# Kernel tuning notes

Measured on AMD Instinct MI355X. Metric: run time of the kernel, lower is better.

Reference implementation:

```python
import jax, jax.numpy as jnp
import numpy as np

B, P, ENC = 64, 196, 512
E, H, A, V, L = 1024, 1024, 512, 20000, 25


def setup_inputs() -> dict:
    key = jax.random.key(0)
    ks = jax.random.split(key, 20)
    s = 0.02
    return {
        "encoder_out": jax.random.normal(ks[0], (B, P, ENC), jnp.float32),
        "captions": jax.random.randint(ks[1], (B, L), 0, V),
        "lengths": L,
        # attention MLP
        "W_enc_att": jax.random.normal(ks[2], (ENC, A), jnp.float32) * s,
        "b_enc_att": jnp.zeros((A,), jnp.float32),
        "W_dec_att": jax.random.normal(ks[3], (H, A), jnp.float32) * s,
        "b_dec_att": jnp.zeros((A,), jnp.float32),
        "W_full_att": jax.random.normal(ks[4], (A, 1), jnp.float32) * s,
        "b_full_att": jnp.zeros((1,), jnp.float32),
        # embedding
        "emb_table": jax.random.normal(ks[5], (V, E), jnp.float32) * s,
        # LSTMCell: input = embedding + context -> (E+ENC, 4H)
        "W_ih": jax.random.normal(ks[6], (E + ENC, 4 * H), jnp.float32) * s,
        "b_ih": jnp.zeros((4 * H,), jnp.float32),
        "W_hh": jax.random.normal(ks[7], (H, 4 * H), jnp.float32) * s,
        "b_hh": jnp.zeros((4 * H,), jnp.float32),
        # init states
        "W_init_h": jax.random.normal(ks[8], (ENC, H), jnp.float32) * s,
        "b_init_h": jnp.zeros((H,), jnp.float32),
        "W_init_c": jax.random.normal(ks[9], (ENC, H), jnp.float32) * s,
        "b_init_c": jnp.zeros((H,), jnp.float32),
        # gate + output proj
        "W_fbeta": jax.random.normal(ks[10], (H, ENC), jnp.float32) * s,
        "b_fbeta": jnp.zeros((ENC,), jnp.float32),
        "W_fc": jax.random.normal(ks[11], (H, V), jnp.float32) * s,
        "b_fc": jnp.zeros((V,), jnp.float32),
    }


def _decode(encoder_out, W_enc_att, b_enc_att, W_dec_att, b_dec_att,
            W_full_att, b_full_att, emb_table, W_ih, b_ih, W_hh, b_hh,
            W_init_h, b_init_h, W_init_c, b_init_c, W_fbeta, b_fbeta,
            W_fc, b_fc, captions, T):
    # precompute encoder-side attention projection (constant across timesteps)
    att_enc = encoder_out @ W_enc_att + b_enc_att          # (B, P, A)
    mean_feat = encoder_out.mean(axis=1)                   # (B, ENC)
    h0 = mean_feat @ W_init_h + b_init_h
    c0 = mean_feat @ W_init_c + b_init_c
    embeddings = emb_table[captions[:, :T]]                # (B, T, E)
    xs = jnp.swapaxes(embeddings, 0, 1)                    # (T, B, E)

    def step(carry, emb_t):
        h, c = carry
        att_dec = h @ W_dec_att + b_dec_att                # (B, A)
        energy = (jax.nn.relu(att_enc + att_dec[:, None, :]) @ W_full_att
                  + b_full_att)[..., 0]                    # (B, P)
        alpha = jax.nn.softmax(energy, axis=1)
        context = jnp.einsum('bp,bpe->be', alpha, encoder_out)
        gate = jax.nn.sigmoid(h @ W_fbeta + b_fbeta)       # (B, ENC)
        x = jnp.concatenate([emb_t, gate * context], axis=1)
        gates = x @ W_ih + b_ih + h @ W_hh + b_hh          # (B, 4H)
        i, f, g, o = jnp.split(gates, 4, axis=1)           # torch order i,f,g,o
        c = jax.nn.sigmoid(f) * c + jax.nn.sigmoid(i) * jnp.tanh(g)
        h = jax.nn.sigmoid(o) * jnp.tanh(c)
        preds = h @ W_fc + b_fc                            # dropout = identity (eval)
        return (h, c), (preds, alpha)

    _, (preds, alphas) = jax.lax.scan(step, (h0, c0), xs)
    predictions = jnp.swapaxes(preds, 0, 1)                # (B, T, V)
    alphas = jnp.swapaxes(alphas, 0, 1)                    # (B, T, P)
    return predictions, alphas


def reference(encoder_out, captions, lengths, W_enc_att, b_enc_att, W_dec_att,
              b_dec_att, W_full_att, b_full_att, emb_table, W_ih, b_ih, W_hh,
              b_hh, W_init_h, b_init_h, W_init_c, b_init_c, W_fbeta, b_fbeta,
              W_fc, b_fc):
    T = int(lengths) - 1
    return _decode(encoder_out, W_enc_att, b_enc_att, W_dec_att, b_dec_att,
                   W_full_att, b_full_att, emb_table, W_ih, b_ih, W_hh, b_hh,
                   W_init_h, b_init_h, W_init_c, b_init_c, W_fbeta, b_fbeta,
                   W_fc, b_fc, captions, T)
```

## Files before the change

kernel.cpp:

```cpp
#include <hip/hip_runtime.h>
#include <hip/hip_bf16.h>

#define BB 64
#define PP 196
#define ENCD 512
#define ED 1024
#define HD 1024
#define AD 512
#define VD 20000
#define TT 24
#define VPAD 20096
#define NS 8

typedef __attribute__((ext_vector_type(8))) short short8;
typedef __attribute__((ext_vector_type(4))) short short4v;
typedef __attribute__((ext_vector_type(4))) float f32x4;

__device__ __forceinline__ unsigned short f2bf(float f) {
    unsigned u = __builtin_bit_cast(unsigned, f);
    u = (u + 0x7FFFu + ((u >> 16) & 1u)) >> 16;
    return (unsigned short)u;
}
__device__ __forceinline__ void split2(float v, unsigned short& h, unsigned short& l) {
    h = f2bf(v);
    float hf = __builtin_bit_cast(float, ((unsigned)h) << 16);
    l = f2bf(v - hf);
}

__global__ __launch_bounds__(256) void split_w_kernel(
    const float* __restrict__ W, unsigned short* __restrict__ oh,
    unsigned short* __restrict__ ol, int N, int Npad, int coff, int Nlaunch) {
    int n = blockIdx.x * 256 + threadIdx.x;
    if (n >= Nlaunch) return;
    int kc = blockIdx.y;
    short8 vh, vl;
    #pragma unroll
    for (int j = 0; j < 8; ++j) {
        float v = (n < N) ? W[(size_t)(kc * 8 + j) * N + n] : 0.f;
        unsigned short h, l; split2(v, h, l);
        vh[j] = (short)h; vl[j] = (short)l;
    }
    size_t o = ((size_t)kc * Npad + coff + n) * 8;
    *(short8*)(oh + o) = vh; *(short8*)(ol + o) = vl;
}

__global__ __launch_bounds__(128) void embed_split_kernel(
    const int* __restrict__ captions, const float* __restrict__ table,
    unsigned short* __restrict__ eh, unsigned short* __restrict__ el) {
    int t = blockIdx.x, b = blockIdx.y;
    int kc = threadIdx.x;
    int tok = captions[b * 25 + t];
    const float* row = table + (size_t)tok * ED;
    short8 vh, vl;
    #pragma unroll
    for (int j = 0; j < 8; ++j) {
        unsigned short h, l; split2(row[kc * 8 + j], h, l);
        vh[j] = (short)h; vl[j] = (short)l;
    }
    size_t o = ((size_t)t * 128 * 64 + (size_t)kc * 64 + b) * 8;
    *(short8*)(eh + o) = vh; *(short8*)(el + o) = vl;
}

__global__ __launch_bounds__(512) void mean_kernel(const float* __restrict__ enc,
                                                   float* __restrict__ mf) {
    int b = blockIdx.x; int e = threadIdx.x;
    const float* base = enc + (size_t)b * PP * ENCD + e;
    float s = 0.f;
    #pragma unroll 4
    for (int p = 0; p < PP; ++p) s += base[(size_t)p * ENCD];
    mf[b * ENCD + e] = s * (1.f / PP);
}

__global__ __launch_bounds__(256) void init_hc_kernel(
    const float* __restrict__ mf,
    const float* __restrict__ Wh, const float* __restrict__ bh,
    const float* __restrict__ Wc, const float* __restrict__ bc,
    unsigned short* __restrict__ hc_h, unsigned short* __restrict__ hc_l,
    float* __restrict__ c0) {
    int b = blockIdx.x;
    int isC = blockIdx.y;
    const float* W    = isC ? Wc : Wh;
    const float* bias = isC ? bc : bh;
    __shared__ float smf[ENCD];
    for (int i = threadIdx.x; i < ENCD; i += 256) smf[i] = mf[b * ENCD + i];
    __syncthreads();
    #pragma unroll
    for (int jj = 0; jj < 4; ++jj) {
        int j = threadIdx.x + jj * 256;
        float acc = bias[j];
        for (int k = 0; k < ENCD; ++k) acc += smf[k] * W[(size_t)k * HD + j];
        if (isC) c0[b * HD + j] = acc;
        else {
            unsigned short h, l; split2(acc, h, l);
            size_t o = ((size_t)(j >> 3) * 64 + b) * 8 + (j & 7);
            hc_h[o] = h; hc_l[o] = l;
        }
    }
}

__global__ __launch_bounds__(256) void mfma_gemm_bigf(
    const float* __restrict__ Ap,
    const unsigned short* __restrict__ Bh, const unsigned short* __restrict__ Bl,
    const float* __restrict__ bias, float* __restrict__ C,
    int N, int Npad, int K, int Mtiles, int Ntiles, int inner_m) {
    __shared__ __align__(16) short lds[32768];
    short* Ahs = lds;
    short* Als = lds + 8192;
    short* Bhs = lds + 16384;
    short* Bls = lds + 24576;
    int tid = threadIdx.x, lane = tid & 63, w = tid >> 6;
    int nwg = Mtiles * Ntiles;
    int orig = blockIdx.x;
    int q = nwg >> 3, r = nwg & 7;
    int xcd = orig & 7;
    int basew = (xcd < r) ? xcd * (q + 1) : r * (q + 1) + (xcd - r) * q;
    int wg = basew + (orig >> 3);
    int mt, nt;
    if (inner_m) { mt = wg % Mtiles; nt = wg / Mtiles; }
    else         { nt = wg % Ntiles; mt = wg / Ntiles; }
    int m0 = mt * 128, n0 = nt * 128;
    int wr = w >> 1, wc = w & 1;
    f32x4 acc[4][4];
    #pragma unroll
    for (int i = 0; i < 4; ++i)
        #pragma unroll
        for (int j = 0; j < 4; ++j) acc[i][j] = (f32x4){0.f, 0.f, 0.f, 0.f};
    int nsteps = K >> 6;
    for (int s = 0; s < nsteps; ++s) {
        int k0 = s * 64, kc0 = s * 8;
        float4 va[8];
        #pragma unroll
        for (int it = 0; it < 8; ++it) {
            int idx = it * 256 + tid; int m = idx >> 4, k4 = idx & 15;
            va[it] = *(const float4*)(Ap + (size_t)(m0 + m) * K + k0 + k4 * 4);
        }
        short8 rb[2][4];
        #pragma unroll
        for (int it = 0; it < 4; ++it) {
            int g = w * 4 + it; int kcl = g >> 1; int rb0 = (g & 1) * 64;
            size_t gb = ((size_t)(kc0 + kcl) * Npad + n0 + rb0 + lane) * 8;
            rb[0][it] = *(const short8*)(Bh + gb);
            rb[1][it] = *(const short8*)(Bl + gb);
        }
        __syncthreads();
        #pragma unroll
        for (int it = 0; it < 8; ++it) {
            int idx = it * 256 + tid; int m = idx >> 4, k4 = idx & 15;
            int kc = k4 >> 1, jh = (k4 & 1) * 4;
            float vv[4] = {va[it].x, va[it].y, va[it].z, va[it].w};
            short4v hv, lv;
            #pragma unroll
            for (int qq = 0; qq < 4; ++qq) {
                unsigned short h, l; split2(vv[qq], h, l);
                hv[qq] = (short)h; lv[qq] = (short)l;
            }
            int o = kc * 1024 + ((m ^ kc) << 3) + jh;
            *(short4v*)(Ahs + o) = hv;
            *(short4v*)(Als + o) = lv;
        }
        #pragma unroll
        for (int it = 0; it < 4; ++it) {
            int g = w * 4 + it; int kcl = g >> 1; int rb0 = (g & 1) * 64;
            int o = (kcl * 128 + rb0 + lane) * 8;
            *(short8*)(Bhs + o) = rb[0][it];
            *(short8*)(Bls + o) = rb[1][it];
        }
        __syncthreads();
        #pragma unroll
        for (int ks = 0; ks < 2; ++ks) {
            int kq = ks * 4 + (lane >> 4);
            short8 afh[4], afl[4], bfh[4], bfl[4];
            #pragma unroll
            for (int mi = 0; mi < 4; ++mi) {
                int row = wr * 64 + mi * 16 + (lane & 15);
                int o = kq * 1024 + ((row ^ kq) << 3);
                afh[mi] = *(const short8*)(Ahs + o);
                afl[mi] = *(const short8*)(Als + o);
            }
            #pragma unroll
            for (int ni = 0; ni < 4; ++ni) {
                int o = (kq * 128 + wc * 64 + ni * 16 + (lane & 15)) * 8;
                bfh[ni] = *(const short8*)(Bhs + o);
                bfl[ni] = *(const short8*)(Bls + o);
            }
            #pragma unroll
            for (int mi = 0; mi < 4; ++mi)
                #pragma unroll
                for (int ni = 0; ni < 4; ++ni) {
                    acc[mi][ni] = __builtin_amdgcn_mfma_f32_16x16x32_bf16(afh[mi], bfh[ni], acc[mi][ni], 0, 0, 0);
                    acc[mi][ni] = __builtin_amdgcn_mfma_f32_16x16x32_bf16(afh[mi], bfl[ni], acc[mi][ni], 0, 0, 0);
                    acc[mi][ni] = __builtin_amdgcn_mfma_f32_16x16x32_bf16(afl[mi], bfh[ni], acc[mi][ni], 0, 0, 0);
                }
        }
    }
    #pragma unroll
    for (int mi = 0; mi < 4; ++mi) {
        int rrow = m0 + wr * 64 + mi * 16 + ((lane >> 4) << 2);
        #pragma unroll
        for (int ni = 0; ni < 4; ++ni) {
            int c = n0 + wc * 64 + ni * 16 + (lane & 15);
            if (c < N) {
                float bv = bias ? bias[c] : 0.f;
                #pragma unroll
                for (int qq = 0; qq < 4; ++qq)
                    C[(size_t)(rrow + qq) * N + c] = acc[mi][ni][qq] + bv;
            }
        }
    }
}

__global__ __launch_bounds__(256) void mfma_gemm_small(
    const unsigned short* __restrict__ A0h, const unsigned short* __restrict__ A0l,
    const unsigned short* __restrict__ A1h, const unsigned short* __restrict__ A1l,
    const unsigned short* __restrict__ A2h, const unsigned short* __restrict__ A2l,
    int c0, int c1,
    const unsigned short* __restrict__ B0h, const unsigned short* __restrict__ B0l,
    const unsigned short* __restrict__ B1h, const unsigned short* __restrict__ B1l,
    int bc0, float* __restrict__ out, int Npad, int steps) {
    __shared__ __align__(16) short lds[24576];
    short* Ahs = lds;
    short* Als = lds + 4096;
    short* Bhs = lds + 8192;
    short* Bls = lds + 16384;
    int tid = threadIdx.x, lane = tid & 63, w = tid >> 6;
    int n0 = blockIdx.x * 128;
    int kc_base = blockIdx.y * steps * 8;
    out += (size_t)blockIdx.y * 64 * Npad;
    f32x4 acc[4][2];
    #pragma unroll
    for (int i = 0; i < 4; ++i)
        #pragma unroll
        for (int j = 0; j < 2; ++j) acc[i][j] = (f32x4){0.f, 0.f, 0.f, 0.f};
    for (int s = 0; s < steps; ++s) {
        int kc0 = kc_base + s * 8;
        short8 raa[2][2], rbb[2][4];
        #pragma unroll
        for (int it = 0; it < 2; ++it) {
            int kcl = w * 2 + it; int kcg = kc0 + kcl;
            const unsigned short *ph, *pl; size_t off;
            if (kcg < c0)       { ph = A0h; pl = A0l; off = ((size_t)kcg * 64 + lane) * 8; }
            else if (kcg < c1)  { ph = A1h; pl = A1l; off = ((size_t)(kcg - c0) * 64 + lane) * 8; }
            else                { ph = A2h; pl = A2l; off = ((size_t)(kcg - c1) * 64 + lane) * 8; }
            raa[0][it] = *(const short8*)(ph + off);
            raa[1][it] = *(const short8*)(pl + off);
        }
        #pragma unroll
        for (int it = 0; it < 4; ++it) {
            int g = w * 4 + it; int kcl = g >> 1; int cb = (g & 1) * 64; int kcg = kc0 + kcl;
            const unsigned short *ph, *pl; size_t off;
            if (kcg < bc0) { ph = B0h; pl = B0l; off = ((size_t)kcg * Npad + n0 + cb + lane) * 8; }
            else           { ph = B1h; pl = B1l; off = ((size_t)(kcg - bc0) * Npad + n0 + cb + lane) * 8; }
            rbb[0][it] = *(const short8*)(ph + off);
            rbb[1][it] = *(const short8*)(pl + off);
        }
        __syncthreads();
        #pragma unroll
        for (int it = 0; it < 2; ++it) {
            int kcl = w * 2 + it; int o = (kcl * 64 + lane) * 8;
            *(short8*)(Ahs + o) = raa[0][it];
            *(short8*)(Als + o) = raa[1][it];
        }
        #pragma unroll
        for (int it = 0; it < 4; ++it) {
            int g = w * 4 + it; int kcl = g >> 1; int cb = (g & 1) * 64;
            int o = (kcl * 128 + cb + lane) * 8;
            *(short8*)(Bhs + o) = rbb[0][it];
            *(short8*)(Bls + o) = rbb[1][it];
        }
        __syncthreads();
        #pragma unroll
        for (int ks = 0; ks < 2; ++ks) {
            int kq = ks * 4 + (lane >> 4);
            short8 afh[4], afl[4], bfh[2], bfl[2];
            #pragma unroll
            for (int mi = 0; mi < 4; ++mi) {
                int o = (kq * 64 + mi * 16 + (lane & 15)) * 8;
                afh[mi] = *(const short8*)(Ahs + o);
                afl[mi] = *(const short8*)(Als + o);
            }
            #pragma unroll
            for (int ni = 0; ni < 2; ++ni) {
                int o = (kq * 128 + w * 32 + ni * 16 + (lane & 15)) * 8;
                bfh[ni] = *(const short8*)(Bhs + o);
                bfl[ni] = *(const short8*)(Bls + o);
            }
            #pragma unroll
            for (int mi = 0; mi < 4; ++mi)
                #pragma unroll
                for (int ni = 0; ni < 2; ++ni) {
                    acc[mi][ni] = __builtin_amdgcn_mfma_f32_16x16x32_bf16(afh[mi], bfh[ni], acc[mi][ni], 0, 0, 0);
                    acc[mi][ni] = __builtin_amdgcn_mfma_f32_16x16x32_bf16(afh[mi], bfl[ni], acc[mi][ni], 0, 0, 0);
                    acc[mi][ni] = __builtin_amdgcn_mfma_f32_16x16x32_bf16(afl[mi], bfh[ni], acc[mi][ni], 0, 0, 0);
                }
        }
        __syncthreads();
    }
    #pragma unroll
    for (int mi = 0; mi < 4; ++mi) {
        int rrow = mi * 16 + ((lane >> 4) << 2);
        #pragma unroll
        for (int ni = 0; ni < 2; ++ni) {
            int c = n0 + w * 32 + ni * 16 + (lane & 15);
            #pragma unroll
            for (int qq = 0; qq < 4; ++qq)
                out[(size_t)(rrow + qq) * Npad + c] = acc[mi][ni][qq];
        }
    }
}

__global__ __launch_bounds__(512) void attn_fused_kernel(
    const float* __restrict__ att_enc, const float* __restrict__ adg,
    const float* __restrict__ b_dec, const float* __restrict__ Wfull,
    const float* __restrict__ enc, const float* __restrict__ b_fbeta,
    float* __restrict__ alpha_out, unsigned short* __restrict__ x2h,
    unsigned short* __restrict__ x2l, int t) {
    int b = blockIdx.x; int tid = threadIdx.x;
    __shared__ float sdec[AD], sw[AD], red[512], sal[PP];
    if (tid < AD) {
        float s = b_dec[tid];
        #pragma unroll
        for (int ks = 0; ks < NS; ++ks) s += adg[((size_t)ks * BB + b) * 1024 + tid];
        sdec[tid] = s;
        sw[tid] = Wfull[tid];
    }
    __syncthreads();
    int p = tid & 255, half = tid >> 8;
    float part = 0.f;
    if (p < PP) {
        const float* row = att_enc + ((size_t)b * PP + p) * AD + half * 256;
        const float* sd = sdec + half * 256;
        const float* swp = sw + half * 256;
        #pragma unroll 4
        for (int a0 = 0; a0 < 256; a0 += 4) {
            float4 v = *(const float4*)(row + a0);
            part += fmaxf(v.x + sd[a0 + 0], 0.f) * swp[a0 + 0];
            part += fmaxf(v.y + sd[a0 + 1], 0.f) * swp[a0 + 1];
            part += fmaxf(v.z + sd[a0 + 2], 0.f) * swp[a0 + 2];
            part += fmaxf(v.w + sd[a0 + 3], 0.f) * swp[a0 + 3];
        }
    }
    red[tid] = part;
    __syncthreads();
    float myE = (tid < PP) ? red[tid] + red[tid + 256] : -1e30f;
    __syncthreads();
    red[tid] = myE;
    __syncthreads();
    for (int s = 256; s > 0; s >>= 1) {
        if (tid < s) red[tid] = fmaxf(red[tid], red[tid + s]);
        __syncthreads();
    }
    float mx = red[0];
    __syncthreads();
    float ex = (tid < PP) ? __expf(myE - mx) : 0.f;
    red[tid] = ex;
    __syncthreads();
    for (int s = 256; s > 0; s >>= 1) {
        if (tid < s) red[tid] += red[tid + s];
        __syncthreads();
    }
    float al = ex * (1.f / red[0]);
    if (tid < PP) {
        sal[tid] = al;
        alpha_out[((size_t)b * TT + t) * PP + tid] = al;
    }
    __syncthreads();
    int e = tid;
    const float* basep = enc + (size_t)b * PP * ENCD + e;
    float s = 0.f;
    #pragma unroll 4
    for (int pp = 0; pp < PP; ++pp) s += sal[pp] * basep[(size_t)pp * ENCD];
    float gpre = b_fbeta[e];
    #pragma unroll
    for (int ks = 0; ks < NS; ++ks) gpre += adg[((size_t)ks * BB + b) * 1024 + AD + e];
    float gate = 1.f / (1.f + __expf(-gpre));
    unsigned short h, l; split2(gate * s, h, l);
    size_t o = ((size_t)(e >> 3) * 64 + b) * 8 + (e & 7);
    x2h[o] = h; x2l[o] = l;
}

__global__ __launch_bounds__(256) void lstm_kernel(
    const float* __restrict__ gp, const float* __restrict__ b_ih,
    const float* __restrict__ b_hh, float* __restrict__ c,
    unsigned short* __restrict__ hc_h, unsigned short* __restrict__ hc_l,
    float* __restrict__ h_all, int t) {
    int b = blockIdx.x; int tid = threadIdx.x;
    #pragma unroll
    for (int jj = 0; jj < 4; ++jj) {
        int j = tid + jj * 256;
        float gi = b_ih[j] + b_hh[j];
        float gf = b_ih[1024 + j] + b_hh[1024 + j];
        float gg = b_ih[2048 + j] + b_hh[2048 + j];
        float go = b_ih[3072 + j] + b_hh[3072 + j];
        #pragma unroll
        for (int ks = 0; ks < NS; ++ks) {
            const float* g = gp + ((size_t)ks * BB + b) * 4096;
            gi += g[j]; gf += g[1024 + j]; gg += g[2048 + j]; go += g[3072 + j];
        }
        float si = 1.f / (1.f + __expf(-gi));
        float sf = 1.f / (1.f + __expf(-gf));
        float so = 1.f / (1.f + __expf(-go));
        float cn = sf * c[b * HD + j] + si * tanhf(gg);
        c[b * HD + j] = cn;
        float hn = so * tanhf(cn);
        unsigned short h, l; split2(hn, h, l);
        size_t o1 = ((size_t)(j >> 3) * 64 + b) * 8 + (j & 7);
        hc_h[o1] = h; hc_l[o1] = l;
        h_all[((size_t)b * TT + t) * HD + j] = hn;
    }
}

extern "C" void kernel_launch(void* const* d_in, const int* in_sizes, int n_in,
                              void* d_out, int out_size, void* d_ws, size_t ws_size,
                              hipStream_t stream) {
    const float* enc      = (const float*)d_in[0];
    const int*   captions = (const int*)d_in[1];
    const float* W_enc    = (const float*)d_in[3];
    const float* b_enc    = (const float*)d_in[4];
    const float* W_dec    = (const float*)d_in[5];
    const float* b_dec    = (const float*)d_in[6];
    const float* W_full   = (const float*)d_in[7];
    const float* table    = (const float*)d_in[9];
    const float* W_ih     = (const float*)d_in[10];
    const float* b_ih     = (const float*)d_in[11];
    const float* W_hh     = (const float*)d_in[12];
    const float* b_hh     = (const float*)d_in[13];
    const float* W_init_h = (const float*)d_in[14];
    const float* b_init_h = (const float*)d_in[15];
    const float* W_init_c = (const float*)d_in[16];
    const float* b_init_c = (const float*)d_in[17];
    const float* W_fbeta  = (const float*)d_in[18];
    const float* b_fbeta  = (const float*)d_in[19];
    const float* W_fc     = (const float*)d_in[20];
    const float* b_fc     = (const float*)d_in[21];

    float* preds  = (float*)d_out;
    float* alphas = (float*)d_out + (size_t)BB * TT * VD;

    char* base = (char*)d_ws;
    size_t off = 0;
    auto take = [&](size_t b) { void* r = (void*)(base + off); off += (b + 255) & ~(size_t)255; return r; };
    float* att_enc = (float*)take((size_t)12544 * 512 * 4);
    unsigned short* wih_h  = (unsigned short*)take((size_t)192 * 4096 * 8 * 2);
    unsigned short* wih_l  = (unsigned short*)take((size_t)192 * 4096 * 8 * 2);
    unsigned short* whh_h  = (unsigned short*)take((size_t)128 * 4096 * 8 * 2);
    unsigned short* whh_l  = (unsigned short*)take((size_t)128 * 4096 * 8 * 2);
    unsigned short* watt_h = (unsigned short*)take((size_t)128 * 1024 * 8 * 2);
    unsigned short* watt_l = (unsigned short*)take((size_t)128 * 1024 * 8 * 2);
    unsigned short* wenc_h = (unsigned short*)take((size_t)64 * 512 * 8 * 2);
    unsigned short* wenc_l = (unsigned short*)take((size_t)64 * 512 * 8 * 2);
    unsigned short* emb_h  = (unsigned short*)take((size_t)TT * 128 * 64 * 8 * 2);
    unsigned short* emb_l  = (unsigned short*)take((size_t)TT * 128 * 64 * 8 * 2);
    float* adg = (float*)take((size_t)NS * BB * 1024 * 4);
    float* gp  = (float*)take((size_t)NS * BB * 4096 * 4);
    unsigned short* wfc_h = (unsigned short*)(base);
    unsigned short* wfc_l = (unsigned short*)(base + (size_t)128 * VPAD * 8 * 2);
    float* c_buf = (float*)take((size_t)BB * HD * 4);
    float* mf    = (float*)take((size_t)BB * ENCD * 4);
    unsigned short* x2c_h = (unsigned short*)take((size_t)64 * 64 * 8 * 2);
    unsigned short* x2c_l = (unsigned short*)take((size_t)64 * 64 * 8 * 2);
    unsigned short* hc_h  = (unsigned short*)take((size_t)128 * 64 * 8 * 2);
    unsigned short* hc_l  = (unsigned short*)take((size_t)128 * 64 * 8 * 2);
    float* h_all = (float*)take((size_t)TT * BB * HD * 4);

    const int BIG = 1 << 20;

    split_w_kernel<<<dim3(2, 64), 256, 0, stream>>>(W_enc, wenc_h, wenc_l, 512, 512, 0, 512);
    split_w_kernel<<<dim3(2, 128), 256, 0, stream>>>(W_dec, watt_h, watt_l, 512, 1024, 0, 512);
    split_w_kernel<<<dim3(2, 128), 256, 0, stream>>>(W_fbeta, watt_h, watt_l, 512, 1024, 512, 512);
    split_w_kernel<<<dim3(16, 192), 256, 0, stream>>>(W_ih, wih_h, wih_l, 4096, 4096, 0, 4096);
    split_w_kernel<<<dim3(16, 128), 256, 0, stream>>>(W_hh, whh_h, whh_l, 4096, 4096, 0, 4096);
    embed_split_kernel<<<dim3(TT, BB), 128, 0, stream>>>(captions, table, emb_h, emb_l);
    mean_kernel<<<BB, 512, 0, stream>>>(enc, mf);
    init_hc_kernel<<<dim3(BB, 2), 256, 0, stream>>>(mf, W_init_h, b_init_h, W_init_c, b_init_c,
                                                    hc_h, hc_l, c_buf);
    mfma_gemm_bigf<<<392, 256, 0, stream>>>(enc, wenc_h, wenc_l, b_enc, att_enc,
                                            512, 512, 512, 98, 4, 0);

    for (int t = 0; t < TT; ++t) {
        mfma_gemm_small<<<dim3(8, NS), 256, 0, stream>>>(
            hc_h, hc_l, nullptr, nullptr, nullptr, nullptr, BIG, BIG,
            watt_h, watt_l, nullptr, nullptr, BIG, adg, 1024, 2);
        attn_fused_kernel<<<BB, 512, 0, stream>>>(att_enc, adg, b_dec, W_full, enc, b_fbeta,
                                                  alphas, x2c_h, x2c_l, t);
        mfma_gemm_small<<<dim3(32, NS), 256, 0, stream>>>(
            emb_h + (size_t)t * 128 * 64 * 8, emb_l + (size_t)t * 128 * 64 * 8,
            x2c_h, x2c_l, hc_h, hc_l, 128, 192,
            wih_h, wih_l, whh_h, whh_l, 192, gp, 4096, 5);
        lstm_kernel<<<BB, 256, 0, stream>>>(gp, b_ih, b_hh, c_buf, hc_h, hc_l, h_all, t);
    }

    split_w_kernel<<<dim3(79, 128), 256, 0, stream>>>(W_fc, wfc_h, wfc_l, VD, VPAD, 0, VPAD);
    mfma_gemm_bigf<<<1884, 256, 0, stream>>>(h_all, wfc_h, wfc_l, b_fc, preds,
                                             VD, VPAD, 1024, 12, 157, 1);
}
```

Measured before the change: 1.834 ms.

## Prefetch next K-step in GEMMs, split attention kernel, widen LSTM grid

Both MFMA GEMM kernels now issue the global loads for the next K step right after the LDS stores, so those loads overlap the current step's MFMAs. The small GEMM also drops its trailing barrier. The fused attention kernel is split in two: an energy/softmax kernel that uses one wavefront per pixel with shuffle reductions, and a context/gate kernel launched on a (B,4) grid for more parallelism. The LSTM kernel goes from a 64-block grid to (64,4). The trade-off is higher register pressure from the prefetch buffers and one extra kernel launch per timestep.

```diff
diff --git a/kernel.cpp b/kernel.cpp
--- a/kernel.cpp
+++ b/kernel.cpp
@@ -126,15 +126,15 @@
         #pragma unroll
         for (int j = 0; j < 4; ++j) acc[i][j] = (f32x4){0.f, 0.f, 0.f, 0.f};
     int nsteps = K >> 6;
-    for (int s = 0; s < nsteps; ++s) {
+    float4 va[8];
+    short8 rb[2][4];
+    auto load_step = [&](int s) {
         int k0 = s * 64, kc0 = s * 8;
-        float4 va[8];
         #pragma unroll
         for (int it = 0; it < 8; ++it) {
             int idx = it * 256 + tid; int m = idx >> 4, k4 = idx & 15;
             va[it] = *(const float4*)(Ap + (size_t)(m0 + m) * K + k0 + k4 * 4);
         }
-        short8 rb[2][4];
         #pragma unroll
         for (int it = 0; it < 4; ++it) {
             int g = w * 4 + it; int kcl = g >> 1; int rb0 = (g & 1) * 64;
@@ -142,6 +142,9 @@
             rb[0][it] = *(const short8*)(Bh + gb);
             rb[1][it] = *(const short8*)(Bl + gb);
         }
+    };
+    load_step(0);
+    for (int s = 0; s < nsteps; ++s) {
         __syncthreads();
         #pragma unroll
         for (int it = 0; it < 8; ++it) {
@@ -166,6 +169,7 @@
             *(short8*)(Bls + o) = rb[1][it];
         }
         __syncthreads();
+        if (s + 1 < nsteps) load_step(s + 1);
         #pragma unroll
         for (int ks = 0; ks < 2; ++ks) {
             int kq = ks * 4 + (lane >> 4);
@@ -231,9 +235,9 @@
     for (int i = 0; i < 4; ++i)
         #pragma unroll
         for (int j = 0; j < 2; ++j) acc[i][j] = (f32x4){0.f, 0.f, 0.f, 0.f};
-    for (int s = 0; s < steps; ++s) {
+    short8 raa[2][2], rbb[2][4];
+    auto load_step = [&](int s) {
         int kc0 = kc_base + s * 8;
-        short8 raa[2][2], rbb[2][4];
         #pragma unroll
         for (int it = 0; it < 2; ++it) {
             int kcl = w * 2 + it; int kcg = kc0 + kcl;
@@ -253,6 +257,9 @@
             rbb[0][it] = *(const short8*)(ph + off);
             rbb[1][it] = *(const short8*)(pl + off);
         }
+    };
+    load_step(0);
+    for (int s = 0; s < steps; ++s) {
         __syncthreads();
         #pragma unroll
         for (int it = 0; it < 2; ++it) {
@@ -268,6 +275,7 @@
             *(short8*)(Bls + o) = rbb[1][it];
         }
         __syncthreads();
+        if (s + 1 < steps) load_step(s + 1);
         #pragma unroll
         for (int ks = 0; ks < 2; ++ks) {
             int kq = ks * 4 + (lane >> 4);
@@ -293,7 +301,6 @@
                     acc[mi][ni] = __builtin_amdgcn_mfma_f32_16x16x32_bf16(afl[mi], bfh[ni], acc[mi][ni], 0, 0, 0);
                 }
         }
-        __syncthreads();
     }
     #pragma unroll
     for (int mi = 0; mi < 4; ++mi) {
@@ -308,14 +315,12 @@
     }
 }
 
-__global__ __launch_bounds__(512) void attn_fused_kernel(
+__global__ __launch_bounds__(1024) void energy_softmax_kernel(
     const float* __restrict__ att_enc, const float* __restrict__ adg,
     const float* __restrict__ b_dec, const float* __restrict__ Wfull,
-    const float* __restrict__ enc, const float* __restrict__ b_fbeta,
-    float* __restrict__ alpha_out, unsigned short* __restrict__ x2h,
-    unsigned short* __restrict__ x2l, int t) {
+    float* __restrict__ alpha_out, int t) {
     int b = blockIdx.x; int tid = threadIdx.x;
-    __shared__ float sdec[AD], sw[AD], red[512], sal[PP];
+    __shared__ float sdec[AD], sw[AD], sE[256], red[256];
     if (tid < AD) {
         float s = b_dec[tid];
         #pragma unroll
@@ -324,51 +329,57 @@
         sw[tid] = Wfull[tid];
     }
     __syncthreads();
-    int p = tid & 255, half = tid >> 8;
-    float part = 0.f;
-    if (p < PP) {
-        const float* row = att_enc + ((size_t)b * PP + p) * AD + half * 256;
-        const float* sd = sdec + half * 256;
-        const float* swp = sw + half * 256;
-        #pragma unroll 4
-        for (int a0 = 0; a0 < 256; a0 += 4) {
-            float4 v = *(const float4*)(row + a0);
-            part += fmaxf(v.x + sd[a0 + 0], 0.f) * swp[a0 + 0];
-            part += fmaxf(v.y + sd[a0 + 1], 0.f) * swp[a0 + 1];
-            part += fmaxf(v.z + sd[a0 + 2], 0.f) * swp[a0 + 2];
-            part += fmaxf(v.w + sd[a0 + 3], 0.f) * swp[a0 + 3];
-        }
-    }
-    red[tid] = part;
-    __syncthreads();
-    float myE = (tid < PP) ? red[tid] + red[tid + 256] : -1e30f;
-    __syncthreads();
-    red[tid] = myE;
-    __syncthreads();
-    for (int s = 256; s > 0; s >>= 1) {
+    int w = tid >> 6, lane = tid & 63;
+    float4 sd0 = *(const float4*)&sdec[lane * 8];
+    float4 sd1 = *(const float4*)&sdec[lane * 8 + 4];
+    float4 sw0 = *(const float4*)&sw[lane * 8];
+    float4 sw1 = *(const float4*)&sw[lane * 8 + 4];
+    for (int p = w; p < PP; p += 16) {
+        const float* row = att_enc + ((size_t)b * PP + p) * AD + lane * 8;
+        float4 v0 = *(const float4*)row;
+        float4 v1 = *(const float4*)(row + 4);
+        float part = fmaxf(v0.x + sd0.x, 0.f) * sw0.x + fmaxf(v0.y + sd0.y, 0.f) * sw0.y +
+                     fmaxf(v0.z + sd0.z, 0.f) * sw0.z + fmaxf(v0.w + sd0.w, 0.f) * sw0.w +
+                     fmaxf(v1.x + sd1.x, 0.f) * sw1.x + fmaxf(v1.y + sd1.y, 0.f) * sw1.y +
+                     fmaxf(v1.z + sd1.z, 0.f) * sw1.z + fmaxf(v1.w + sd1.w, 0.f) * sw1.w;
+        #pragma unroll
+        for (int off = 32; off > 0; off >>= 1) part += __shfl_down(part, off, 64);
+        if (lane == 0) sE[p] = part;
+    }
+    __syncthreads();
+    float myE = (tid < PP) ? sE[tid] : -1e30f;
+    if (tid < 256) red[tid] = myE;
+    __syncthreads();
+    for (int s = 128; s > 0; s >>= 1) {
         if (tid < s) red[tid] = fmaxf(red[tid], red[tid + s]);
         __syncthreads();
     }
     float mx = red[0];
     __syncthreads();
     float ex = (tid < PP) ? __expf(myE - mx) : 0.f;
-    red[tid] = ex;
-    __syncthreads();
-    for (int s = 256; s > 0; s >>= 1) {
+    if (tid < 256) red[tid] = ex;
+    __syncthreads();
+    for (int s = 128; s > 0; s >>= 1) {
         if (tid < s) red[tid] += red[tid + s];
         __syncthreads();
     }
-    float al = ex * (1.f / red[0]);
-    if (tid < PP) {
-        sal[tid] = al;
-        alpha_out[((size_t)b * TT + t) * PP + tid] = al;
-    }
-    __syncthreads();
-    int e = tid;
+    if (tid < PP) alpha_out[((size_t)b * TT + t) * PP + tid] = ex * (1.f / red[0]);
+}
+
+__global__ __launch_bounds__(128) void context_gate_kernel(
+    const float* __restrict__ enc, const float* __restrict__ alpha,
+    const float* __restrict__ adg, const float* __restrict__ b_fbeta,
+    unsigned short* __restrict__ x2h, unsigned short* __restrict__ x2l, int t) {
+    int b = blockIdx.x;
+    int e = blockIdx.y * 128 + threadIdx.x;
+    __shared__ float sal[PP];
+    for (int i = threadIdx.x; i < PP; i += 128)
+        sal[i] = alpha[((size_t)b * TT + t) * PP + i];
+    __syncthreads();
     const float* basep = enc + (size_t)b * PP * ENCD + e;
     float s = 0.f;
     #pragma unroll 4
-    for (int pp = 0; pp < PP; ++pp) s += sal[pp] * basep[(size_t)pp * ENCD];
+    for (int p = 0; p < PP; ++p) s += sal[p] * basep[(size_t)p * ENCD];
     float gpre = b_fbeta[e];
     #pragma unroll
     for (int ks = 0; ks < NS; ++ks) gpre += adg[((size_t)ks * BB + b) * 1024 + AD + e];
@@ -383,30 +394,27 @@
     const float* __restrict__ b_hh, float* __restrict__ c,
     unsigned short* __restrict__ hc_h, unsigned short* __restrict__ hc_l,
     float* __restrict__ h_all, int t) {
-    int b = blockIdx.x; int tid = threadIdx.x;
-    #pragma unroll
-    for (int jj = 0; jj < 4; ++jj) {
-        int j = tid + jj * 256;
-        float gi = b_ih[j] + b_hh[j];
-        float gf = b_ih[1024 + j] + b_hh[1024 + j];
-        float gg = b_ih[2048 + j] + b_hh[2048 + j];
-        float go = b_ih[3072 + j] + b_hh[3072 + j];
-        #pragma unroll
-        for (int ks = 0; ks < NS; ++ks) {
-            const float* g = gp + ((size_t)ks * BB + b) * 4096;
-            gi += g[j]; gf += g[1024 + j]; gg += g[2048 + j]; go += g[3072 + j];
-        }
-        float si = 1.f / (1.f + __expf(-gi));
-        float sf = 1.f / (1.f + __expf(-gf));
-        float so = 1.f / (1.f + __expf(-go));
-        float cn = sf * c[b * HD + j] + si * tanhf(gg);
-        c[b * HD + j] = cn;
-        float hn = so * tanhf(cn);
-        unsigned short h, l; split2(hn, h, l);
-        size_t o1 = ((size_t)(j >> 3) * 64 + b) * 8 + (j & 7);
-        hc_h[o1] = h; hc_l[o1] = l;
-        h_all[((size_t)b * TT + t) * HD + j] = hn;
-    }
+    int b = blockIdx.x;
+    int j = blockIdx.y * 256 + threadIdx.x;
+    float gi = b_ih[j] + b_hh[j];
+    float gf = b_ih[1024 + j] + b_hh[1024 + j];
+    float gg = b_ih[2048 + j] + b_hh[2048 + j];
+    float go = b_ih[3072 + j] + b_hh[3072 + j];
+    #pragma unroll
+    for (int ks = 0; ks < NS; ++ks) {
+        const float* g = gp + ((size_t)ks * BB + b) * 4096;
+        gi += g[j]; gf += g[1024 + j]; gg += g[2048 + j]; go += g[3072 + j];
+    }
+    float si = 1.f / (1.f + __expf(-gi));
+    float sf = 1.f / (1.f + __expf(-gf));
+    float so = 1.f / (1.f + __expf(-go));
+    float cn = sf * c[b * HD + j] + si * tanhf(gg);
+    c[b * HD + j] = cn;
+    float hn = so * tanhf(cn);
+    unsigned short h, l; split2(hn, h, l);
+    size_t o1 = ((size_t)(j >> 3) * 64 + b) * 8 + (j & 7);
+    hc_h[o1] = h; hc_l[o1] = l;
+    h_all[((size_t)b * TT + t) * HD + j] = hn;
 }
 
 extern "C" void kernel_launch(void* const* d_in, const int* in_sizes, int n_in,
@@ -480,13 +488,14 @@
         mfma_gemm_small<<<dim3(8, NS), 256, 0, stream>>>(
             hc_h, hc_l, nullptr, nullptr, nullptr, nullptr, BIG, BIG,
             watt_h, watt_l, nullptr, nullptr, BIG, adg, 1024, 2);
-        attn_fused_kernel<<<BB, 512, 0, stream>>>(att_enc, adg, b_dec, W_full, enc, b_fbeta,
-                                                  alphas, x2c_h, x2c_l, t);
+        energy_softmax_kernel<<<BB, 1024, 0, stream>>>(att_enc, adg, b_dec, W_full, alphas, t);
+        context_gate_kernel<<<dim3(BB, 4), 128, 0, stream>>>(enc, alphas, adg, b_fbeta,
+                                                             x2c_h, x2c_l, t);
         mfma_gemm_small<<<dim3(32, NS), 256, 0, stream>>>(
             emb_h + (size_t)t * 128 * 64 * 8, emb_l + (size_t)t * 128 * 64 * 8,
             x2c_h, x2c_l, hc_h, hc_l, 128, 192,
             wih_h, wih_l, whh_h, whh_l, 192, gp, 4096, 5);
-        lstm_kernel<<<BB, 256, 0, stream>>>(gp, b_ih, b_hh, c_buf, hc_h, hc_l, h_all, t);
+        lstm_kernel<<<dim3(BB, 4), 256, 0, stream>>>(gp, b_ih, b_hh, c_buf, hc_h, hc_l, h_all, t);
     }
 
     split_w_kernel<<<dim3(79, 128), 256, 0, stream>>>(W_fc, wfc_h, wfc_l, VD, VPAD, 0, VPAD);
```

New measurement: 1.514 ms. 17.5% less time.
